# Performance work log

Measured on AMD Instinct MI355X. Metric: run time of the kernel, lower is better.

## Reference

```python
import jax, jax.numpy as jnp
import numpy as np
from jax import lax

B, N, FEAT, MID, HID, OUT = 128, 36, 2048, 517, 128, 1024
STEPS, TEMP = 3, 1.0


def setup_inputs() -> dict:
    key = jax.random.key(0)
    ks = jax.random.split(key, 10)
    s = 0.02
    return {
        "boxes": jax.random.uniform(ks[0], (B, 4, N), jnp.float32),
        "attention": jax.random.normal(ks[1], (B, N), jnp.float32),
        "features": jax.random.normal(ks[2], (B, N, FEAT), jnp.float32),
        "conv_w": jax.random.normal(ks[3], (MID - 5, FEAT), jnp.float32) * s,
        "conv_b": jnp.zeros((MID - 5,), jnp.float32),
        "skew_wx": jax.random.normal(ks[4], (HID, MID), jnp.float32) * s,
        "skew_wy": jax.random.normal(ks[5], (HID, MID), jnp.float32) * s,
        "skew_b1": jnp.zeros((HID,), jnp.float32),
        "skew_w2": jax.random.normal(ks[6], (HID,), jnp.float32) * s,
        "skew_b2": jnp.zeros((1,), jnp.float32),
        "w_ih": jax.random.normal(ks[7], (4 * OUT, MID), jnp.float32) * s,
        "w_hh": jax.random.normal(ks[8], (4 * OUT, OUT), jnp.float32) * s,
        "b_ih": jnp.zeros((4 * OUT,), jnp.float32),
        "b_hh": jnp.zeros((4 * OUT,), jnp.float32),
        "lr": jnp.ones((1,), jnp.float32),
    }


def _calculate_assignment(C, lr_abs, temp, steps):
    # C: (b, n, n) skew-symmetric ordering costs.
    logits = jnp.zeros_like(C)
    for _ in range(steps):
        P = jax.nn.softmax(logits / temp, axis=-1)  # position i -> distribution over elements l
        cum = jnp.cumsum(P, axis=1)                 # sum over positions k <= i
        below = cum - P                             # sum_{k<i} P_kl
        above = cum[:, -1:, :] - cum                # sum_{k>i} P_kl
        # grad_{ij} = sum_l C_{jl} * (above - below)_{il}  (uses skew-symmetry of C)
        G = jnp.einsum('bil,bjl->bij', above - below, C)
        logits = logits - lr_abs * G
    return jax.nn.softmax(logits / temp, axis=-1)


def reference(boxes, attention, features, conv_w, conv_b, skew_wx, skew_wy,
              skew_b1, skew_w2, skew_b2, w_ih, w_hh, b_ih, b_hh, lr):
    b = boxes.shape[0]
    # normalize boxes by per-sample max
    boxes = boxes / jnp.max(boxes.reshape(b, -1), axis=1)[:, None, None]
    # pointwise Conv1: 2048 -> MID-5, features arrives as (b, n, 2048)
    f = jnp.einsum('bnf,mf->bmn', features, conv_w) + conv_b[None, :, None]
    att = attention[:, None, :]                      # (b, 1, n)
    feats = jnp.concatenate([boxes, att, f], axis=1)  # (b, MID, n)
    # PairwiseSkew: f(x_i, x_j) - f(x_j, x_i); the first 1x1-conv over concatenated
    # pairs splits into two linear maps so we never materialize (b, 2*MID, n, n).
    hx = jnp.einsum('hm,bmn->bhn', skew_wx, feats)
    hy = jnp.einsum('hm,bmn->bhn', skew_wy, feats)
    h = jax.nn.relu(hx[:, :, :, None] + hy[:, :, None, :] + skew_b1[None, :, None, None])
    out = jnp.einsum('h,bhij->bij', skew_w2, h) + skew_b2[0]  # (b, n, n)
    C = out - jnp.swapaxes(out, 1, 2)  # skew-symmetrize
    A = _calculate_assignment(C, jnp.abs(lr)[0], TEMP, STEPS)
    # gate features by sigmoid(attention) and apply soft permutation
    gated = feats * jax.nn.sigmoid(att)               # (b, MID, n)
    x = jnp.einsum('bcl,bil->bci', gated, A)          # (b, MID, n)
    x_seq = jnp.transpose(x, (2, 0, 1))               # (n, b, MID)
    # single-layer LSTM (PyTorch gate order i, f, g, o); return final cell state
    bias = b_ih + b_hh
    Hd = w_hh.shape[1]
    def step(carry, xt):
        h_, c_ = carry
        gates = xt @ w_ih.T + h_ @ w_hh.T + bias
        i, fg, g, o = jnp.split(gates, 4, axis=-1)
        c_ = jax.nn.sigmoid(fg) * c_ + jax.nn.sigmoid(i) * jnp.tanh(g)
        h_ = jax.nn.sigmoid(o) * jnp.tanh(c_)
        return (h_, c_), None
    init = (jnp.zeros((b, Hd), x.dtype), jnp.zeros((b, Hd), x.dtype))
    (_, c_fin), _ = lax.scan(step, init, x_seq)
    return c_fin
```

## Files before the change

### kernel.cpp

```cpp
#include <hip/hip_runtime.h>
#include <math.h>

#define NB 128
#define NN 36
#define S37 37
#define S40 40
#define NFEAT 2048
#define NMID 517
#define KP 544
#define NHID 128
#define NOUT 1024
#define ROWS (NB*NN)

typedef __bf16 bf16x8 __attribute__((ext_vector_type(8)));
typedef float  f32x4  __attribute__((ext_vector_type(4)));

__device__ __forceinline__ float sigf(float x){ return 1.f/(1.f+expf(-x)); }
__device__ __forceinline__ unsigned short f2bf(float x){
    unsigned u = __float_as_uint(x);
    return (unsigned short)((u + 0x7FFFu + ((u>>16)&1u)) >> 16);
}
__device__ __forceinline__ float bf2f(unsigned short b){
    return __uint_as_float(((unsigned)b) << 16);
}

__global__ __launch_bounds__(256) void prep_all(
    const float* __restrict__ boxes, const float* __restrict__ att,
    const float* __restrict__ features, const float* __restrict__ conv_w,
    const float* __restrict__ wx, const float* __restrict__ wy,
    const float* __restrict__ b1, const float* __restrict__ w_ih,
    const float* __restrict__ w_hh, const float* __restrict__ b_ih,
    const float* __restrict__ b_hh,
    unsigned short* __restrict__ features_bf, unsigned short* __restrict__ convw_bf,
    unsigned short* __restrict__ wxy_bf, float* __restrict__ hxy_b,
    unsigned short* __restrict__ wih_il, unsigned short* __restrict__ whh_il,
    float* __restrict__ comb_b, unsigned int* __restrict__ bar,
    float* __restrict__ feats)
{
    int gtid = blockIdx.x*256 + threadIdx.x;
    int gs = gridDim.x*256;
    if (gtid < 128*64) {
        int b = gtid >> 6, t = gtid & 63;
        float mx = -1e30f;
        for (int idx = t; idx < 4*NN; idx += 64) mx = fmaxf(mx, boxes[b*4*NN + idx]);
        for (int off = 32; off > 0; off >>= 1) mx = fmaxf(mx, __shfl_down(mx, off));
        mx = __shfl(mx, 0);
        float inv = 1.f / mx;
        for (int idx = t; idx < 4*NN; idx += 64) {
            int r = idx / NN, n = idx - r*NN;
            feats[(size_t)(b*NN+n)*NMID + r] = boxes[b*4*NN + idx] * inv;
        }
        if (t < NN) feats[(size_t)(b*NN+t)*NMID + 4] = att[b*NN + t];
    }
    for (int i = gtid; i < ROWS*NFEAT; i += gs) features_bf[i] = f2bf(features[i]);
    for (int i = gtid; i < 512*NFEAT; i += gs) convw_bf[i] = f2bf(conv_w[i]);
    for (int i = gtid; i < 256*KP; i += gs) {
        int r = i / KP, k = i - r*KP;
        float v = 0.f;
        if (k < NMID) v = (r < NHID) ? wx[(size_t)r*NMID+k] : wy[(size_t)(r-NHID)*NMID+k];
        wxy_bf[i] = f2bf(v);
    }
    for (int i = gtid; i < 256; i += gs) hxy_b[i] = (i < NHID) ? b1[i] : 0.f;
    for (int i = gtid; i < 4*NOUT*KP; i += gs) {
        int row = i / KP, k = i - row*KP;
        int u = row >> 2, g = row & 3;
        wih_il[i] = (k < NMID) ? f2bf(w_ih[(size_t)(g*NOUT+u)*NMID + k]) : (unsigned short)0;
    }
    for (int i = gtid; i < 4*NOUT*NOUT; i += gs) {
        int row = i >> 10, k = i & 1023;
        int u = row >> 2, g = row & 3;
        whh_il[i] = f2bf(w_hh[(size_t)(g*NOUT+u)*NOUT + k]);
    }
    for (int i = gtid; i < 4*NOUT; i += gs) {
        int u = i >> 2, g = i & 3;
        comb_b[i] = b_ih[g*NOUT+u] + b_hh[g*NOUT+u];
    }
    for (int i = gtid; i < 512; i += gs) bar[i] = 0u;
}

__global__ __launch_bounds__(256) void gemm128(
    const unsigned short* __restrict__ A, const unsigned short* __restrict__ B,
    const float* __restrict__ bias, void* __restrict__ Cp,
    int Ksl, int lda, int ldb, int ldc, int obf, long long pstride)
{
    __shared__ __align__(16) char As[16384];
    __shared__ __align__(16) char Bs[16384];
    int m0 = blockIdx.y * 128, n0 = blockIdx.x * 128;
    int kbeg = blockIdx.z * Ksl;
    int tid = threadIdx.x;
    int lane = tid & 63, wave = tid >> 6;
    int wm = wave >> 1, wn = wave & 1;
    int sw = ((lane>>4)<<8) + (((lane&15) ^ ((lane>>4)<<2))<<4);
    f32x4 acc[4][4];
    #pragma unroll
    for (int i = 0; i < 4; ++i)
        #pragma unroll
        for (int j = 0; j < 4; ++j) acc[i][j] = (f32x4){0.f,0.f,0.f,0.f};

    for (int k0 = 0; k0 < Ksl; k0 += 32) {
        #pragma unroll
        for (int p = 0; p < 2; ++p) {
            int cc = p*256 + tid;
            int r = cc >> 2, q = cc & 3;
            int sa = ((r>>4)<<10) + (q<<8) + ((((r&15) ^ (q<<2)))<<4);
            uint4 va = *(const uint4*)(A + (size_t)(m0+r)*lda + kbeg + k0 + q*8);
            *(uint4*)(As + sa) = va;
            uint4 vb = *(const uint4*)(B + (size_t)(n0+r)*ldb + kbeg + k0 + q*8);
            *(uint4*)(Bs + sa) = vb;
        }
        __syncthreads();
        bf16x8 af[4], bfr[4];
        #pragma unroll
        for (int i = 0; i < 4; ++i) af[i]  = *(bf16x8*)(As + ((wm*4+i)<<10) + sw);
        #pragma unroll
        for (int j = 0; j < 4; ++j) bfr[j] = *(bf16x8*)(Bs + ((wn*4+j)<<10) + sw);
        #pragma unroll
        for (int i = 0; i < 4; ++i)
            #pragma unroll
            for (int j = 0; j < 4; ++j)
                acc[i][j] = __builtin_amdgcn_mfma_f32_16x16x32_bf16(af[i], bfr[j], acc[i][j], 0, 0, 0);
        __syncthreads();
    }
    int colf = lane & 15, rowq = lane >> 4;
    #pragma unroll
    for (int j = 0; j < 4; ++j) {
        int col = n0 + (wn*4+j)*16 + colf;
        float bv = bias ? bias[col] : 0.f;
        #pragma unroll
        for (int i = 0; i < 4; ++i) {
            #pragma unroll
            for (int reg = 0; reg < 4; ++reg) {
                int row = m0 + (wm*4+i)*16 + rowq*4 + reg;
                float v = acc[i][j][reg] + bv;
                if (obf) ((unsigned short*)Cp)[(size_t)row*ldc + col] = f2bf(v);
                else ((float*)Cp + (size_t)blockIdx.z*pstride)[(size_t)row*ldc + col] = v;
            }
        }
    }
}

__global__ __launch_bounds__(256) void conv_reduce(
    const float* __restrict__ part, const float* __restrict__ bias,
    float* __restrict__ feats, unsigned short* __restrict__ feats_bf)
{
    int gtid = blockIdx.x*256 + threadIdx.x;
    int gs = gridDim.x*256;
    const size_t PS = (size_t)ROWS * 512;
    for (int i = gtid; i < ROWS*512; i += gs) {
        int r = i >> 9, cc = i & 511;
        float s = part[i] + part[PS+i] + part[2*PS+i] + part[3*PS+i] + bias[cc];
        feats[(size_t)r*NMID + 5 + cc] = s;
        feats_bf[(size_t)r*KP + 5 + cc] = f2bf(s);
    }
    for (int i = gtid; i < ROWS*5; i += gs) {
        int r = i / 5, cc = i - r*5;
        feats_bf[(size_t)r*KP + cc] = f2bf(feats[(size_t)r*NMID + cc]);
    }
    for (int i = gtid; i < ROWS*27; i += gs) {
        int r = i / 27, cc = i - r*27;
        feats_bf[(size_t)r*KP + 517 + cc] = 0;
    }
}

__global__ __launch_bounds__(256) void gemm_mfma(
    const unsigned short* __restrict__ A, const unsigned short* __restrict__ B,
    const float* __restrict__ bias, void* __restrict__ Cp,
    int K, int lda, int ldb, int ldc, int obf)
{
    __shared__ __align__(16) char As[8192];
    __shared__ __align__(16) char Bs[4096];
    int m0 = blockIdx.y * 128, n0 = blockIdx.x * 64;
    int tid = threadIdx.x;
    int lane = tid & 63, wave = tid >> 6;
    int wm = wave >> 1, wn = wave & 1;
    f32x4 acc[4][2];
    #pragma unroll
    for (int i = 0; i < 4; ++i)
        #pragma unroll
        for (int j = 0; j < 2; ++j) acc[i][j] = (f32x4){0.f,0.f,0.f,0.f};

    for (int k0 = 0; k0 < K; k0 += 32) {
        #pragma unroll
        for (int cc = tid; cc < 512; cc += 256) {
            int r = cc >> 2, q = cc & 3;
            uint4 v = *(const uint4*)(A + (size_t)(m0+r)*lda + k0 + q*8);
            *(uint4*)(As + ((r>>4)<<10) + (q<<8) + ((r&15)<<4)) = v;
        }
        {
            int r = tid >> 2, q = tid & 3;
            uint4 v = *(const uint4*)(B + (size_t)(n0+r)*ldb + k0 + q*8);
            *(uint4*)(Bs + ((r>>4)<<10) + (q<<8) + ((r&15)<<4)) = v;
        }
        __syncthreads();
        bf16x8 af[4], bfr[2];
        #pragma unroll
        for (int i = 0; i < 4; ++i) af[i]  = *(bf16x8*)(As + ((wm*4+i)<<10) + (lane<<4));
        #pragma unroll
        for (int j = 0; j < 2; ++j) bfr[j] = *(bf16x8*)(Bs + ((wn*2+j)<<10) + (lane<<4));
        #pragma unroll
        for (int i = 0; i < 4; ++i)
            #pragma unroll
            for (int j = 0; j < 2; ++j)
                acc[i][j] = __builtin_amdgcn_mfma_f32_16x16x32_bf16(af[i], bfr[j], acc[i][j], 0, 0, 0);
        __syncthreads();
    }
    int colf = lane & 15, rowq = lane >> 4;
    #pragma unroll
    for (int j = 0; j < 2; ++j) {
        int col = n0 + (wn*2+j)*16 + colf;
        float bv = bias ? bias[col] : 0.f;
        #pragma unroll
        for (int i = 0; i < 4; ++i) {
            #pragma unroll
            for (int reg = 0; reg < 4; ++reg) {
                int row = m0 + (wm*4+i)*16 + rowq*4 + reg;
                float v = acc[i][j][reg] + bv;
                if (obf) ((unsigned short*)Cp)[(size_t)row*ldc + col] = f2bf(v);
                else     ((float*)Cp)[(size_t)row*ldc + col] = v;
            }
        }
    }
}

__global__ __launch_bounds__(256) void out_k(
    const float* __restrict__ hxy, const float* __restrict__ w2,
    float* __restrict__ out_g)
{
    __shared__ float s_hx[9*129], s_hy[NN*129], s_w2[NHID];
    int b = blockIdx.x, i0 = blockIdx.y * 9, tid = threadIdx.x;
    for (int i = tid; i < 9*NHID; i += 256) {
        int n = i >> 7, h = i & 127;
        s_hx[n*129+h] = hxy[(size_t)(b*NN+i0+n)*256 + h];
    }
    for (int i = tid; i < NN*NHID; i += 256) {
        int n = i >> 7, h = i & 127;
        s_hy[n*129+h] = hxy[(size_t)(b*NN+n)*256 + 128 + h];
    }
    if (tid < NHID) s_w2[tid] = w2[tid];
    __syncthreads();
    for (int idx = tid; idx < 9*NN; idx += 256) {
        int il = idx / NN, j = idx - il*NN;
        const float* px = &s_hx[il*129];
        const float* py = &s_hy[j*129];
        float s = 0.f;
        #pragma unroll 8
        for (int h = 0; h < NHID; ++h) s += s_w2[h] * fmaxf(px[h] + py[h], 0.f);
        out_g[(size_t)b*NN*NN + (i0+il)*NN + j] = s;
    }
}

__global__ __launch_bounds__(256) void iter_k(
    const float* __restrict__ out_g, const float* __restrict__ att,
    const float* __restrict__ lr, float* __restrict__ A_g)
{
    __shared__ __align__(16) float s_out[NN*S40], s_C[NN*S40], s_logits[NN*S40], s_P[NN*S40];
    __shared__ float s_sg[NN];
    int b = blockIdx.x, tid = threadIdx.x;
    for (int idx = tid; idx < NN*NN; idx += 256) {
        int i = idx / NN, j = idx - i*NN;
        s_out[i*S40+j] = out_g[(size_t)b*NN*NN + idx];
        s_logits[i*S40+j] = 0.f;
    }
    if (tid < NN) s_sg[tid] = sigf(att[b*NN + tid]);
    float lr_abs = fabsf(lr[0]);
    __syncthreads();
    for (int idx = tid; idx < NN*NN; idx += 256) {
        int i = idx / NN, j = idx - i*NN;
        s_C[i*S40+j] = s_out[i*S40+j] - s_out[j*S40+i];
    }
    __syncthreads();
    for (int it = 0; it < 3; ++it) {
        if (tid < NN) {
            int i = tid;
            float mx = -1e30f;
            for (int l = 0; l < NN; ++l) mx = fmaxf(mx, s_logits[i*S40+l]);
            float sum = 0.f;
            for (int l = 0; l < NN; ++l) { float e = expf(s_logits[i*S40+l]-mx); s_P[i*S40+l] = e; sum += e; }
            float inv = 1.f/sum;
            for (int l = 0; l < NN; ++l) s_P[i*S40+l] *= inv;
        }
        __syncthreads();
        if (tid < NN) {
            int l = tid;
            float S = 0.f;
            for (int i = 0; i < NN; ++i) S += s_P[i*S40+l];
            float cum = 0.f;
            for (int i = 0; i < NN; ++i) {
                float p = s_P[i*S40+l];
                cum += p;
                s_P[i*S40+l] = S - 2.f*cum + p;
            }
        }
        __syncthreads();
        for (int idx = tid; idx < NN*NN; idx += 256) {
            int i = idx / NN, j = idx - i*NN;
            const f32x4* Pp = (const f32x4*)&s_P[i*S40];
            const f32x4* Cc = (const f32x4*)&s_C[j*S40];
            float g = 0.f;
            #pragma unroll
            for (int q = 0; q < 9; ++q) {
                f32x4 a = Pp[q], bb = Cc[q];
                g += a[0]*bb[0] + a[1]*bb[1] + a[2]*bb[2] + a[3]*bb[3];
            }
            s_logits[i*S40+j] -= lr_abs * g;
        }
        __syncthreads();
    }
    if (tid < NN) {
        int i = tid;
        float mx = -1e30f;
        for (int l = 0; l < NN; ++l) mx = fmaxf(mx, s_logits[i*S40+l]);
        float sum = 0.f;
        for (int l = 0; l < NN; ++l) { float e = expf(s_logits[i*S40+l]-mx); s_P[i*S40+l] = e; sum += e; }
        float inv = 1.f/sum;
        for (int l = 0; l < NN; ++l)
            A_g[(size_t)b*NN*NN + i*NN + l] = s_P[i*S40+l] * inv * s_sg[l];
    }
}

__global__ __launch_bounds__(256) void xseq_k(
    const float* __restrict__ feats, const float* __restrict__ A_g,
    unsigned short* __restrict__ xseq)
{
    __shared__ float s_P[NN*S37];
    int b = blockIdx.x, half = blockIdx.y, tid = threadIdx.x;
    for (int idx = tid; idx < NN*NN; idx += 256) {
        int i = idx / NN, l = idx - i*NN;
        s_P[i*S37+l] = A_g[(size_t)b*NN*NN + idx];
    }
    __syncthreads();
    const float* fb = feats + (size_t)b*NN*NMID;
    int ncols = (half == 0 && tid < 32) ? 2 : 1;
    #pragma unroll
    for (int rep = 0; rep < 2; ++rep) {
        if (rep >= ncols) break;
        int c = (rep == 0) ? half*256 + tid : 512 + tid;
        float colv[NN];
        #pragma unroll
        for (int l = 0; l < NN; ++l) colv[l] = (c < NMID) ? fb[l*NMID + c] : 0.f;
        #pragma unroll 4
        for (int i = 0; i < NN; ++i) {
            float s = 0.f;
            #pragma unroll
            for (int l = 0; l < NN; ++l) s += s_P[i*S37+l] * colv[l];
            xseq[((size_t)i*NB + b)*KP + c] = f2bf(s);
        }
    }
}

__global__ __launch_bounds__(256, 2) void lstm_persist(
    const unsigned short* __restrict__ whh, const unsigned short* __restrict__ xw,
    unsigned short* __restrict__ hseq, float* __restrict__ dout,
    unsigned int* __restrict__ bar)
{
    __shared__ __align__(16) char Bls[65536];
    __shared__ __align__(16) float gates[32][36];
    int tid = threadIdx.x, lane = tid & 63, wave = tid >> 6;
    int bt = blockIdx.x >> 7, ct = blockIdx.x & 127;
    int m0 = bt * 32, n0 = ct * 32;
    #pragma unroll
    for (int r = 0; r < 16; ++r) {
        int idx = r*256 + tid;
        int n = idx >> 7, kc = idx & 127;
        uint4 v = *(const uint4*)(whh + (size_t)(n0+n)*NOUT + kc*8);
        *(uint4*)(Bls + kc*512 + (((n&16) | ((n^kc)&15))<<4)) = v;
    }
    int wm = wave >> 1, wn = wave & 1;
    int q = lane >> 4, ml = lane & 15;
    int nl = wn*16 + ml;
    int ul = tid & 7, bl = tid >> 3;
    int b = m0 + bl, u = ct*8 + ul;
    unsigned int* flags = bar + bt*128;
    int fidx = lane & 31;
    float cc = 0.f;
    __syncthreads();
    for (int t = 0; t < NN; ++t) {
        uint2 xw2 = *(const uint2*)(xw + ((size_t)t*NB + b)*4*NOUT + n0 + ul*4);
        float g0 = bf2f((unsigned short)(xw2.x & 0xffffu));
        float g1 = bf2f((unsigned short)(xw2.x >> 16));
        float g2 = bf2f((unsigned short)(xw2.y & 0xffffu));
        float g3 = bf2f((unsigned short)(xw2.y >> 16));
        if (t > 0) {
            const unsigned short* hrow = hseq + (size_t)(t-1)*NB*NOUT
                                       + (size_t)(m0 + wm*16 + ml)*NOUT + q*8;
            f32x4 acc = (f32x4){0.f,0.f,0.f,0.f};
            unsigned tgt = (unsigned)t;
            #pragma unroll
            for (int c = 0; c < 4; ++c) {
                for (;;) {
                    unsigned f = __hip_atomic_load(flags + 32*c + fidx,
                                      __ATOMIC_RELAXED, __HIP_MEMORY_SCOPE_AGENT);
                    if (__all(f >= tgt)) break;
                    __builtin_amdgcn_s_sleep(1);
                }
                asm volatile("" ::: "memory");
                #pragma unroll
                for (int it2 = 0; it2 < 8; ++it2) {
                    int it = c*8 + it2;
                    int kc = it*4 + q;
                    bf16x8 a = *(const bf16x8*)(hrow + it*32);
                    bf16x8 bb = *(const bf16x8*)(Bls + kc*512 + (((nl&16) | ((nl^kc)&15))<<4));
                    acc = __builtin_amdgcn_mfma_f32_16x16x32_bf16(a, bb, acc, 0, 0, 0);
                }
            }
            #pragma unroll
            for (int reg = 0; reg < 4; ++reg)
                gates[wm*16 + q*4 + reg][wn*16 + ml] = acc[reg];
            __syncthreads();
            float4 gl = *(const float4*)&gates[bl][ul*4];
            g0 += gl.x; g1 += gl.y; g2 += gl.z; g3 += gl.w;
        }
        float ig = sigf(g0), fg = sigf(g1), gg = tanhf(g2), og = sigf(g3);
        cc = fg*cc + ig*gg;
        if (t == NN-1) {
            dout[(size_t)b*NOUT + u] = cc;
        } else {
            unsigned short hb = f2bf(og*tanhf(cc));
            unsigned partner = (unsigned)__shfl_down((int)(unsigned)hb, 1);
            if ((ul & 1) == 0) {
                unsigned word = (unsigned)hb | (partner << 16);
                unsigned* dst = (unsigned*)(hseq + (size_t)t*NB*NOUT
                                            + (size_t)b*NOUT + u);
                __hip_atomic_store(dst, word, __ATOMIC_RELAXED,
                                   __HIP_MEMORY_SCOPE_AGENT);
            }
            asm volatile("s_waitcnt vmcnt(0)" ::: "memory");
            __syncthreads();
            if (tid == 0)
                __hip_atomic_store(flags + ct, (unsigned)(t + 1),
                                   __ATOMIC_RELAXED, __HIP_MEMORY_SCOPE_AGENT);
        }
    }
}

extern "C" void kernel_launch(void* const* d_in, const int* in_sizes, int n_in,
                              void* d_out, int out_size, void* d_ws, size_t ws_size,
                              hipStream_t stream) {
    (void)in_sizes; (void)n_in; (void)out_size; (void)ws_size;
    const float* boxes     = (const float*)d_in[0];
    const float* attention = (const float*)d_in[1];
    const float* features  = (const float*)d_in[2];
    const float* conv_w    = (const float*)d_in[3];
    const float* conv_b    = (const float*)d_in[4];
    const float* skew_wx   = (const float*)d_in[5];
    const float* skew_wy   = (const float*)d_in[6];
    const float* skew_b1   = (const float*)d_in[7];
    const float* skew_w2   = (const float*)d_in[8];
    const float* w_ih      = (const float*)d_in[10];
    const float* w_hh      = (const float*)d_in[11];
    const float* b_ih      = (const float*)d_in[12];
    const float* b_hh      = (const float*)d_in[13];
    const float* lr        = (const float*)d_in[14];

    char* ws = (char*)d_ws;
    float*          part     = (float*)(ws);
    unsigned short* xw_bf    = (unsigned short*)(ws);
    unsigned short* features_bf = (unsigned short*)(ws + 37748736);
    unsigned short* hseq     = (unsigned short*)(ws + 37748736);
    unsigned short* convw_bf = (unsigned short*)(ws + 56623104);
    float*          feats    = (float*)(ws + 58720256);
    float*          hxy      = (float*)(ws + 68249600);
    unsigned short* feats_bf = (unsigned short*)(ws + 72968192);
    unsigned short* xseq_bf  = (unsigned short*)(ws + 77981696);
    unsigned short* wih_il   = (unsigned short*)(ws + 82995200);
    unsigned short* whh_il   = (unsigned short*)(ws + 87451648);
    unsigned short* wxy_bf   = (unsigned short*)(ws + 95840256);
    float*          comb_b   = (float*)(ws + 96118784);
    float*          hxy_b    = (float*)(ws + 96135168);
    float*          out_g    = (float*)(ws + 96660480);
    float*          A_g      = (float*)(ws + 97324032);
    unsigned int*   bar      = (unsigned int*)(ws + 97987584);

    prep_all<<<2048, 256, 0, stream>>>(boxes, attention, features, conv_w,
                                       skew_wx, skew_wy, skew_b1, w_ih, w_hh,
                                       b_ih, b_hh, features_bf, convw_bf,
                                       wxy_bf, hxy_b, wih_il, whh_il, comb_b,
                                       bar, feats);
    gemm128<<<dim3(4, 36, 4), 256, 0, stream>>>(features_bf, convw_bf, nullptr,
                                                (void*)part, 512, NFEAT, NFEAT, 512, 0,
                                                (long long)ROWS*512);
    conv_reduce<<<2048, 256, 0, stream>>>(part, conv_b, feats, feats_bf);
    gemm_mfma<<<dim3(4, 36), 256, 0, stream>>>(feats_bf, wxy_bf, hxy_b,
                                               (void*)hxy, KP, KP, KP, 256, 0);
    out_k<<<dim3(NB, 4), 256, 0, stream>>>(hxy, skew_w2, out_g);
    iter_k<<<NB, 256, 0, stream>>>(out_g, attention, lr, A_g);
    xseq_k<<<dim3(NB, 2), 256, 0, stream>>>(feats, A_g, xseq_bf);
    gemm128<<<dim3(32, 36, 1), 256, 0, stream>>>(xseq_bf, wih_il, comb_b,
                                                 (void*)xw_bf, KP, KP, KP, 4*NOUT, 1, 0);
    lstm_persist<<<512, 256, 0, stream>>>(whh_il, xw_bf, hseq,
                                          (float*)d_out, bar);
}
```

Measured before the change: 646.6 us.

## Replace split-K conv GEMM and reduce kernel with a fused 64x64 tile GEMM

The pointwise conv previously ran as a 128x128-tile split-K GEMM writing four fp32 partial buffers, followed by a separate reduce kernel that summed them, added bias and wrote the fp32 and bf16 feature copies. It now uses a 64x64-tile GEMM over the full K=2048 that adds bias and writes both outputs directly. The box/attention bf16 columns and the zero padding move into the prep kernel. This removes the partial-sum traffic and one launch, but the new kernel has no software pipelining, a smaller tile with less reuse, and a long serial K loop per block (576 blocks).

New measurement: 665.6 us. +2.9%, slower.

```diff
diff --git a/kernel.cpp b/kernel.cpp
--- a/kernel.cpp
+++ b/kernel.cpp
@@ -35,7 +35,7 @@
     unsigned short* __restrict__ wxy_bf, float* __restrict__ hxy_b,
     unsigned short* __restrict__ wih_il, unsigned short* __restrict__ whh_il,
     float* __restrict__ comb_b, unsigned int* __restrict__ bar,
-    float* __restrict__ feats)
+    float* __restrict__ feats, unsigned short* __restrict__ feats_bf)
 {
     int gtid = blockIdx.x*256 + threadIdx.x;
     int gs = gridDim.x*256;
@@ -48,9 +48,19 @@
         float inv = 1.f / mx;
         for (int idx = t; idx < 4*NN; idx += 64) {
             int r = idx / NN, n = idx - r*NN;
-            feats[(size_t)(b*NN+n)*NMID + r] = boxes[b*4*NN + idx] * inv;
-        }
-        if (t < NN) feats[(size_t)(b*NN+t)*NMID + 4] = att[b*NN + t];
+            float v = boxes[b*4*NN + idx] * inv;
+            feats[(size_t)(b*NN+n)*NMID + r] = v;
+            feats_bf[(size_t)(b*NN+n)*KP + r] = f2bf(v);
+        }
+        if (t < NN) {
+            float av = att[b*NN + t];
+            feats[(size_t)(b*NN+t)*NMID + 4] = av;
+            feats_bf[(size_t)(b*NN+t)*KP + 4] = f2bf(av);
+        }
+    }
+    for (int i = gtid; i < ROWS*27; i += gs) {
+        int r = i / 27, cc = i - r*27;
+        feats_bf[(size_t)r*KP + 517 + cc] = 0;
     }
     for (int i = gtid; i < ROWS*NFEAT; i += gs) features_bf[i] = f2bf(features[i]);
     for (int i = gtid; i < 512*NFEAT; i += gs) convw_bf[i] = f2bf(conv_w[i]);
@@ -76,6 +86,62 @@
         comb_b[i] = b_ih[g*NOUT+u] + b_hh[g*NOUT+u];
     }
     for (int i = gtid; i < 512; i += gs) bar[i] = 0u;
+}
+
+__global__ __launch_bounds__(256) void conv64(
+    const unsigned short* __restrict__ A, const unsigned short* __restrict__ B,
+    const float* __restrict__ bias, float* __restrict__ feats,
+    unsigned short* __restrict__ feats_bf)
+{
+    __shared__ __align__(16) char As[4096];
+    __shared__ __align__(16) char Bs[4096];
+    int n0 = blockIdx.x * 64, m0 = blockIdx.y * 64;
+    int tid = threadIdx.x;
+    int lane = tid & 63, wave = tid >> 6;
+    int wm = wave >> 1, wn = wave & 1;
+    f32x4 acc[2][2];
+    #pragma unroll
+    for (int i = 0; i < 2; ++i)
+        #pragma unroll
+        for (int j = 0; j < 2; ++j) acc[i][j] = (f32x4){0.f,0.f,0.f,0.f};
+
+    int r = tid >> 2, q = tid & 3;
+    const unsigned short* Arow = A + (size_t)(m0+r)*NFEAT + q*8;
+    const unsigned short* Brow = B + (size_t)(n0+r)*NFEAT + q*8;
+    int sa = ((r>>4)<<10) + (q<<8) + ((r&15)<<4);
+
+    for (int k0 = 0; k0 < NFEAT; k0 += 32) {
+        *(uint4*)(As + sa) = *(const uint4*)(Arow + k0);
+        *(uint4*)(Bs + sa) = *(const uint4*)(Brow + k0);
+        __syncthreads();
+        bf16x8 af[2], bfr[2];
+        #pragma unroll
+        for (int i = 0; i < 2; ++i) af[i]  = *(bf16x8*)(As + ((wm*2+i)<<10) + (lane<<4));
+        #pragma unroll
+        for (int j = 0; j < 2; ++j) bfr[j] = *(bf16x8*)(Bs + ((wn*2+j)<<10) + (lane<<4));
+        #pragma unroll
+        for (int i = 0; i < 2; ++i)
+            #pragma unroll
+            for (int j = 0; j < 2; ++j)
+                acc[i][j] = __builtin_amdgcn_mfma_f32_16x16x32_bf16(af[i], bfr[j], acc[i][j], 0, 0, 0);
+        __syncthreads();
+    }
+    int colf = lane & 15, rowq = lane >> 4;
+    #pragma unroll
+    for (int j = 0; j < 2; ++j) {
+        int col = n0 + (wn*2+j)*16 + colf;
+        float bv = bias[col];
+        #pragma unroll
+        for (int i = 0; i < 2; ++i) {
+            #pragma unroll
+            for (int reg = 0; reg < 4; ++reg) {
+                int row = m0 + (wm*2+i)*16 + rowq*4 + reg;
+                float v = acc[i][j][reg] + bv;
+                feats[(size_t)row*NMID + 5 + col] = v;
+                feats_bf[(size_t)row*KP + 5 + col] = f2bf(v);
+            }
+        }
+    }
 }
 
 __global__ __launch_bounds__(256) void gemm128(
@@ -136,29 +202,6 @@
                 else ((float*)Cp + (size_t)blockIdx.z*pstride)[(size_t)row*ldc + col] = v;
             }
         }
-    }
-}
-
-__global__ __launch_bounds__(256) void conv_reduce(
-    const float* __restrict__ part, const float* __restrict__ bias,
-    float* __restrict__ feats, unsigned short* __restrict__ feats_bf)
-{
-    int gtid = blockIdx.x*256 + threadIdx.x;
-    int gs = gridDim.x*256;
-    const size_t PS = (size_t)ROWS * 512;
-    for (int i = gtid; i < ROWS*512; i += gs) {
-        int r = i >> 9, cc = i & 511;
-        float s = part[i] + part[PS+i] + part[2*PS+i] + part[3*PS+i] + bias[cc];
-        feats[(size_t)r*NMID + 5 + cc] = s;
-        feats_bf[(size_t)r*KP + 5 + cc] = f2bf(s);
-    }
-    for (int i = gtid; i < ROWS*5; i += gs) {
-        int r = i / 5, cc = i - r*5;
-        feats_bf[(size_t)r*KP + cc] = f2bf(feats[(size_t)r*NMID + cc]);
-    }
-    for (int i = gtid; i < ROWS*27; i += gs) {
-        int r = i / 27, cc = i - r*27;
-        feats_bf[(size_t)r*KP + 517 + cc] = 0;
     }
 }
 
@@ -453,7 +496,6 @@
     const float* lr        = (const float*)d_in[14];
 
     char* ws = (char*)d_ws;
-    float*          part     = (float*)(ws);
     unsigned short* xw_bf    = (unsigned short*)(ws);
     unsigned short* features_bf = (unsigned short*)(ws + 37748736);
     unsigned short* hseq     = (unsigned short*)(ws + 37748736);
@@ -475,11 +517,9 @@
                                        skew_wx, skew_wy, skew_b1, w_ih, w_hh,
                                        b_ih, b_hh, features_bf, convw_bf,
                                        wxy_bf, hxy_b, wih_il, whh_il, comb_b,
-                                       bar, feats);
-    gemm128<<<dim3(4, 36, 4), 256, 0, stream>>>(features_bf, convw_bf, nullptr,
-                                                (void*)part, 512, NFEAT, NFEAT, 512, 0,
-                                                (long long)ROWS*512);
-    conv_reduce<<<2048, 256, 0, stream>>>(part, conv_b, feats, feats_bf);
+                                       bar, feats, feats_bf);
+    conv64<<<dim3(8, 72), 256, 0, stream>>>(features_bf, convw_bf, conv_b,
+                                            feats, feats_bf);
     gemm_mfma<<<dim3(4, 36), 256, 0, stream>>>(feats_bf, wxy_bf, hxy_b,
                                                (void*)hxy, KP, KP, KP, 256, 0);
     out_k<<<dim3(NB, 4), 256, 0, stream>>>(hxy, skew_w2, out_g);
```
